# Performance work log

Measured on AMD Instinct MI355X. Metric: run time of the kernel, lower is better.

Reference implementation:

```python
import jax, jax.numpy as jnp
import numpy as np

N_ATOMS = 131072
N_MOLS = 4096
D = 128
N_DEPTH = 128
EPS = 1e-07
MEMBERSHIPS = np.array([(-1.645, 0.283), (-1.08, 0.17), (-0.739, 0.134), (-0.468, 0.118),
                        (-0.228, 0.114), (0.0, 0.114), (0.228, 0.114), (0.468, 0.118),
                        (0.739, 0.134), (1.08, 0.17), (1.645, 0.283)], dtype=np.float32)


def setup_inputs() -> dict:
    key = jax.random.key(0)
    k1, k2, k3, k4 = jax.random.split(key, 4)
    x = jax.random.normal(k1, (N_ATOMS, D), dtype=jnp.float32)
    atom_split = jnp.sort(jax.random.randint(k2, (N_ATOMS,), 0, N_MOLS)).astype(jnp.int64)
    W = jax.random.normal(k3, (D * 11, N_DEPTH), dtype=jnp.float32) * 0.02
    b = jax.random.normal(k4, (N_DEPTH,), dtype=jnp.float32) * 0.02
    return {"x": x, "atom_split": atom_split, "W": W, "b": b}


def reference(x, atom_split, W, b):
    means = jnp.asarray(MEMBERSHIPS[:, 0])          # [11]
    stds = jnp.asarray(MEMBERSHIPS[:, 1])           # [11]
    log_norm = jnp.log(stds * np.sqrt(2.0 * np.pi)) # [11]
    # Normal log_prob: -0.5*((x-m)/s)^2 - log(s*sqrt(2pi)); dist_max = log_prob(m) = -log_norm
    z = (x[:, :, None] - means) / stds              # [N, D, 11]
    logp = -0.5 * z * z - log_norm
    out = logp / (-log_norm)                        # divide by log_prob at mean
    out = (out + EPS) / (jnp.sum(out, axis=2, keepdims=True) + EPS)
    out = out.reshape(-1, D * 11)                   # [N, D*11]
    mols = jax.ops.segment_sum(out, atom_split, num_segments=N_MOLS)  # [M, D*11]
    return jnp.tanh(mols @ W + b)                   # [M, n_depth]
```

## Files before the change

### kernel.cpp

```cpp
#include <hip/hip_runtime.h>
#include <math.h>

#define N_ATOMS 131072
#define N_MOLS  4096
#define DFEAT   128
#define NK      11
#define KDIM3   384
#define N_DEPTH 128
#define EPS_F   1e-7f
#define MPB     4

__constant__ float c_means[NK] = {-1.645f, -1.08f, -0.739f, -0.468f, -0.228f,
                                  0.0f, 0.228f, 0.468f, 0.739f, 1.08f, 1.645f};
__constant__ float c_stds[NK]  = {0.283f, 0.17f, 0.134f, 0.118f, 0.114f,
                                  0.114f, 0.114f, 0.118f, 0.134f, 0.17f, 0.283f};


__global__ __launch_bounds__(256) void wxform_offsets_kernel(
    const float* __restrict__ W,
    const int*   __restrict__ split,
    float*       __restrict__ Bt,
    int*         __restrict__ offsets) {
  const int bid = blockIdx.x;
  const int tid = threadIdx.x;
  if (bid < 192) {
    int t = bid * 256 + tid;
    int n = t & 127;
    int row = t >> 7;
    int j = row >> 7;
    int d = row & 127;
    float acc = 0.0f;
#pragma unroll
    for (int k = 0; k < NK; ++k) {
      float m = c_means[k], s = c_stds[k];
      float a = 0.5f / (s * s * logf(s * 2.5066282746310002f));
      float coef = (j == 2) ? a
                 : (j == 1) ? (-2.0f * a * m)
                            : fmaf(a, m * m, 1.0f + EPS_F);
      acc = fmaf(coef, W[(size_t)(d * NK + k) * N_DEPTH + n], acc);
    }
    Bt[(size_t)row * N_DEPTH + n] = acc;
  } else {
    int t = (bid - 192) * 256 + tid;
    if (t <= N_MOLS) {
      int lo = 0, hi = N_ATOMS;
      while (lo < hi) { int mid = (lo + hi) >> 1; if (split[mid] < t) lo = mid + 1; else hi = mid; }
      offsets[t] = lo;
    }
  }
}

__global__ __launch_bounds__(256) void fused_sums_gemm_kernel(
    const float* __restrict__ x,
    const int*   __restrict__ offsets,
    const float* __restrict__ Bt,
    const float* __restrict__ bias,
    float*       __restrict__ out) {
  const int tid = threadIdx.x;
  const int m0  = blockIdx.x * MPB;

  __shared__ float As[MPB][KDIM3];
  __shared__ float red[8][32][13];
  float (*comb)[MPB][DFEAT] = (float (*)[MPB][DFEAT])red;

  float C2 = 0.0f, C1 = 0.0f, C0 = 11.0f + EPS_F;
#pragma unroll
  for (int k = 0; k < NK; ++k) {
    float m_ = c_means[k], s_ = c_stds[k];
    float a = 0.5f / (s_ * s_ * logf(s_ * 2.5066282746310002f));
    C2 += a;
    C1 = fmaf(-2.0f * a, m_, C1);
    C0 = fmaf(a, m_ * m_, C0);
  }

  int offs[MPB + 1];
#pragma unroll
  for (int i = 0; i <= MPB; ++i) offs[i] = offsets[m0 + i];

  const int fq = tid & 31;
  const int g  = tid >> 5;

  for (int i = 0; i < MPB; ++i) {
    float Sr[4]   = {0.f, 0.f, 0.f, 0.f};
    float Sxr[4]  = {0.f, 0.f, 0.f, 0.f};
    float Sxxr[4] = {0.f, 0.f, 0.f, 0.f};

    for (int a = offs[i] + g; a < offs[i + 1]; a += 8) {
      float4 v = *(const float4*)&x[(size_t)a * DFEAT + fq * 4];
      float xv[4] = {v.x, v.y, v.z, v.w};
#pragma unroll
      for (int q = 0; q < 4; ++q) {
        float den = fmaf(fmaf(C2, xv[q], C1), xv[q], C0);
        float r   = __builtin_amdgcn_rcpf(den);
        float u   = xv[q] * r;
        Sr[q]  += r;
        Sxr[q] += u;
        Sxxr[q] = fmaf(xv[q], u, Sxxr[q]);
      }
    }

#pragma unroll
    for (int q = 0; q < 4; ++q) {
      red[g][fq][q * 3 + 0] = Sr[q];
      red[g][fq][q * 3 + 1] = Sxr[q];
      red[g][fq][q * 3 + 2] = Sxxr[q];
    }
    __syncthreads();

    for (int t = tid; t < KDIM3; t += 256) {
      int j = t >> 7;
      int f = t & 127;
      int q = f >> 2, fi = f & 3;
      float s = 0.0f;
#pragma unroll
      for (int gg = 0; gg < 8; ++gg) s += red[gg][q][fi * 3 + j];
      As[i][t] = s;
    }
    __syncthreads();
  }

  const int n = tid & 127;
  const int h = tid >> 7;
  const int kbase = h * (KDIM3 / 2);

  float acc[MPB] = {0.f, 0.f, 0.f, 0.f};
  for (int kk = 0; kk < KDIM3 / 2; kk += 4) {
    int k = kbase + kk;
    float b0 = Bt[(size_t)(k + 0) * N_DEPTH + n];
    float b1 = Bt[(size_t)(k + 1) * N_DEPTH + n];
    float b2 = Bt[(size_t)(k + 2) * N_DEPTH + n];
    float b3 = Bt[(size_t)(k + 3) * N_DEPTH + n];
#pragma unroll
    for (int i = 0; i < MPB; ++i) {
      float4 av = *(const float4*)&As[i][k];
      acc[i] = fmaf(av.x, b0, acc[i]);
      acc[i] = fmaf(av.y, b1, acc[i]);
      acc[i] = fmaf(av.z, b2, acc[i]);
      acc[i] = fmaf(av.w, b3, acc[i]);
    }
  }

#pragma unroll
  for (int i = 0; i < MPB; ++i) comb[h][i][n] = acc[i];
  __syncthreads();

#pragma unroll
  for (int off = 0; off < (MPB * DFEAT) / 256; ++off) {
    int idx = off * 256 + tid;
    int i  = idx >> 7;
    int nn = idx & 127;
    float v = comb[0][i][nn] + comb[1][i][nn] + bias[nn];
    out[(size_t)(m0 + i) * N_DEPTH + nn] = tanhf(v);
  }
}

extern "C" void kernel_launch(void* const* d_in, const int* in_sizes, int n_in,
                              void* d_out, int out_size, void* d_ws, size_t ws_size,
                              hipStream_t stream) {
  const float* x     = (const float*)d_in[0];
  const int*   split = (const int*)d_in[1];
  const float* W     = (const float*)d_in[2];
  const float* bias  = (const float*)d_in[3];
  float* out = (float*)d_out;

  float* Bt      = (float*)d_ws;
  int*   offsets = (int*)((char*)d_ws + (size_t)KDIM3 * N_DEPTH * 4);

  wxform_offsets_kernel<<<dim3(192 + 17), dim3(256), 0, stream>>>(W, split, Bt, offsets);
  fused_sums_gemm_kernel<<<dim3(N_MOLS / MPB), dim3(256), 0, stream>>>(x, offsets, Bt, bias, out);
}
```

Baseline: 119.1 us.

## Process eight molecules per block with a flat atom loop and predicated accumulation

Raises molecules per block from 4 to 8 and replaces the per-molecule atom loop with one flat loop over all atoms of the block's molecules. Each atom is routed to its molecule by comparing its index against the segment offsets, then accumulated into a per-thread register array of 8x12 partial sums. Loads are unrolled by two to expose more memory parallelism, and launch bounds request two blocks per CU. The aim is to remove the short, unbalanced per-molecule loops and the barriers between them, and to reuse each Bt load across more molecules. The cost is heavy register pressure, per-atom select or branch work across eight accumulators, and half as many blocks to spread over the GPU.

```diff
diff --git a/kernel.cpp b/kernel.cpp
--- a/kernel.cpp
+++ b/kernel.cpp
@@ -8,7 +8,7 @@
 #define KDIM3   384
 #define N_DEPTH 128
 #define EPS_F   1e-7f
-#define MPB     4
+#define MPB     8
 
 __constant__ float c_means[NK] = {-1.645f, -1.08f, -0.739f, -0.468f, -0.228f,
                                   0.0f, 0.228f, 0.468f, 0.739f, 1.08f, 1.645f};
@@ -50,7 +50,7 @@
   }
 }
 
-__global__ __launch_bounds__(256) void fused_sums_gemm_kernel(
+__global__ __launch_bounds__(256, 2) void fused_sums_gemm_kernel(
     const float* __restrict__ x,
     const int*   __restrict__ offsets,
     const float* __restrict__ Bt,
@@ -80,40 +80,62 @@
   const int fq = tid & 31;
   const int g  = tid >> 5;
 
-  for (int i = 0; i < MPB; ++i) {
-    float Sr[4]   = {0.f, 0.f, 0.f, 0.f};
-    float Sxr[4]  = {0.f, 0.f, 0.f, 0.f};
-    float Sxxr[4] = {0.f, 0.f, 0.f, 0.f};
+  float acc[MPB][12];
+#pragma unroll
+  for (int i = 0; i < MPB; ++i)
+#pragma unroll
+    for (int j = 0; j < 12; ++j) acc[i][j] = 0.0f;
 
-    for (int a = offs[i] + g; a < offs[i + 1]; a += 8) {
-      float4 v = *(const float4*)&x[(size_t)a * DFEAT + fq * 4];
-      float xv[4] = {v.x, v.y, v.z, v.w};
+  const int base = offs[0], endA = offs[MPB];
+
+  auto proc = [&](float4 v, int a) {
+    float xv[4] = {v.x, v.y, v.z, v.w};
+    float rr[4], uu[4];
 #pragma unroll
-      for (int q = 0; q < 4; ++q) {
-        float den = fmaf(fmaf(C2, xv[q], C1), xv[q], C0);
-        float r   = __builtin_amdgcn_rcpf(den);
-        float u   = xv[q] * r;
-        Sr[q]  += r;
-        Sxr[q] += u;
-        Sxxr[q] = fmaf(xv[q], u, Sxxr[q]);
+    for (int q = 0; q < 4; ++q) {
+      float den = fmaf(fmaf(C2, xv[q], C1), xv[q], C0);
+      rr[q] = __builtin_amdgcn_rcpf(den);
+      uu[q] = xv[q] * rr[q];
+    }
+    int mid = 0;
+#pragma unroll
+    for (int j = 1; j < MPB; ++j) mid += (a >= offs[j]) ? 1 : 0;
+#pragma unroll
+    for (int i = 0; i < MPB; ++i)
+      if (mid == i) {
+#pragma unroll
+        for (int q = 0; q < 4; ++q) {
+          acc[i][3 * q + 0] += rr[q];
+          acc[i][3 * q + 1] += uu[q];
+          acc[i][3 * q + 2] = fmaf(xv[q], uu[q], acc[i][3 * q + 2]);
+        }
       }
-    }
+  };
+
+  int a = base + g;
+  for (; a + 8 < endA; a += 16) {
+    float4 v0 = *(const float4*)&x[(size_t)a * DFEAT + fq * 4];
+    float4 v1 = *(const float4*)&x[(size_t)(a + 8) * DFEAT + fq * 4];
+    proc(v0, a);
+    proc(v1, a + 8);
+  }
+  if (a < endA) {
+    float4 v = *(const float4*)&x[(size_t)a * DFEAT + fq * 4];
+    proc(v, a);
+  }
 
 #pragma unroll
-    for (int q = 0; q < 4; ++q) {
-      red[g][fq][q * 3 + 0] = Sr[q];
-      red[g][fq][q * 3 + 1] = Sxr[q];
-      red[g][fq][q * 3 + 2] = Sxxr[q];
-    }
+  for (int i = 0; i < MPB; ++i) {
+#pragma unroll
+    for (int j = 0; j < 12; ++j) red[g][fq][j] = acc[i][j];
     __syncthreads();
-
     for (int t = tid; t < KDIM3; t += 256) {
-      int j = t >> 7;
+      int comp = t >> 7;
       int f = t & 127;
       int q = f >> 2, fi = f & 3;
       float s = 0.0f;
 #pragma unroll
-      for (int gg = 0; gg < 8; ++gg) s += red[gg][q][fi * 3 + j];
+      for (int gg = 0; gg < 8; ++gg) s += red[gg][q][fi * 3 + comp];
       As[i][t] = s;
     }
     __syncthreads();
@@ -123,7 +145,11 @@
   const int h = tid >> 7;
   const int kbase = h * (KDIM3 / 2);
 
-  float acc[MPB] = {0.f, 0.f, 0.f, 0.f};
+  float pacc[MPB];
+#pragma unroll
+  for (int i = 0; i < MPB; ++i) pacc[i] = 0.0f;
+
+#pragma unroll 2
   for (int kk = 0; kk < KDIM3 / 2; kk += 4) {
     int k = kbase + kk;
     float b0 = Bt[(size_t)(k + 0) * N_DEPTH + n];
@@ -133,15 +159,15 @@
 #pragma unroll
     for (int i = 0; i < MPB; ++i) {
       float4 av = *(const float4*)&As[i][k];
-      acc[i] = fmaf(av.x, b0, acc[i]);
-      acc[i] = fmaf(av.y, b1, acc[i]);
-      acc[i] = fmaf(av.z, b2, acc[i]);
-      acc[i] = fmaf(av.w, b3, acc[i]);
+      pacc[i] = fmaf(av.x, b0, pacc[i]);
+      pacc[i] = fmaf(av.y, b1, pacc[i]);
+      pacc[i] = fmaf(av.z, b2, pacc[i]);
+      pacc[i] = fmaf(av.w, b3, pacc[i]);
     }
   }
 
 #pragma unroll
-  for (int i = 0; i < MPB; ++i) comb[h][i][n] = acc[i];
+  for (int i = 0; i < MPB; ++i) comb[h][i][n] = pacc[i];
   __syncthreads();
 
 #pragma unroll
```

New measurement: 184.2 us. 54.6% more time.

## Assign one wavefront per molecule and reduce sums with shuffles instead of LDS

Applied to the files above, without the earlier changes.

The fused kernel now runs 512 threads handling 8 molecules per block. Each 64-lane wavefront owns one molecule, with the two half-waves taking alternating atoms and the loop unrolled by two. The per-molecule loop of LDS reductions with two block barriers each is replaced by a single cross-half shuffle and one barrier. The GEMM phase splits K four ways across the block. This removes barrier-heavy serial per-molecule reduction, but makes load balance depend on each molecule's atom count and raises register and block-size pressure.

```diff
diff --git a/kernel.cpp b/kernel.cpp
--- a/kernel.cpp
+++ b/kernel.cpp
@@ -8,7 +8,8 @@
 #define KDIM3   384
 #define N_DEPTH 128
 #define EPS_F   1e-7f
-#define MPB     4
+#define MPB     8
+#define TPB     512
 
 __constant__ float c_means[NK] = {-1.645f, -1.08f, -0.739f, -0.468f, -0.228f,
                                   0.0f, 0.228f, 0.468f, 0.739f, 1.08f, 1.645f};
@@ -50,7 +51,7 @@
   }
 }
 
-__global__ __launch_bounds__(256) void fused_sums_gemm_kernel(
+__global__ __launch_bounds__(TPB) void fused_sums_gemm_kernel(
     const float* __restrict__ x,
     const int*   __restrict__ offsets,
     const float* __restrict__ Bt,
@@ -60,8 +61,7 @@
   const int m0  = blockIdx.x * MPB;
 
   __shared__ float As[MPB][KDIM3];
-  __shared__ float red[8][32][13];
-  float (*comb)[MPB][DFEAT] = (float (*)[MPB][DFEAT])red;
+  __shared__ float comb[4][MPB][DFEAT];
 
   float C2 = 0.0f, C1 = 0.0f, C0 = 11.0f + EPS_F;
 #pragma unroll
@@ -73,58 +73,76 @@
     C0 = fmaf(a, m_ * m_, C0);
   }
 
-  int offs[MPB + 1];
+  const int w    = tid >> 6;
+  const int lane = tid & 63;
+  const int fq   = lane & 31;
+  const int h    = lane >> 5;
+
+  const int start = offsets[m0 + w];
+  const int end   = offsets[m0 + w + 1];
+
+  float Sr[4]   = {0.f, 0.f, 0.f, 0.f};
+  float Sxr[4]  = {0.f, 0.f, 0.f, 0.f};
+  float Sxxr[4] = {0.f, 0.f, 0.f, 0.f};
+
+  int a = start + h;
+  for (; a + 2 < end; a += 4) {
+    float4 v0 = *(const float4*)&x[(size_t)a * DFEAT + fq * 4];
+    float4 v1 = *(const float4*)&x[(size_t)(a + 2) * DFEAT + fq * 4];
+    float xv0[4] = {v0.x, v0.y, v0.z, v0.w};
+    float xv1[4] = {v1.x, v1.y, v1.z, v1.w};
 #pragma unroll
-  for (int i = 0; i <= MPB; ++i) offs[i] = offsets[m0 + i];
-
-  const int fq = tid & 31;
-  const int g  = tid >> 5;
-
-  for (int i = 0; i < MPB; ++i) {
-    float Sr[4]   = {0.f, 0.f, 0.f, 0.f};
-    float Sxr[4]  = {0.f, 0.f, 0.f, 0.f};
-    float Sxxr[4] = {0.f, 0.f, 0.f, 0.f};
-
-    for (int a = offs[i] + g; a < offs[i + 1]; a += 8) {
-      float4 v = *(const float4*)&x[(size_t)a * DFEAT + fq * 4];
-      float xv[4] = {v.x, v.y, v.z, v.w};
+    for (int q = 0; q < 4; ++q) {
+      float den0 = fmaf(fmaf(C2, xv0[q], C1), xv0[q], C0);
+      float den1 = fmaf(fmaf(C2, xv1[q], C1), xv1[q], C0);
+      float r0 = __builtin_amdgcn_rcpf(den0);
+      float r1 = __builtin_amdgcn_rcpf(den1);
+      float u0 = xv0[q] * r0;
+      float u1 = xv1[q] * r1;
+      Sr[q]  += r0 + r1;
+      Sxr[q] += u0 + u1;
+      Sxxr[q] = fmaf(xv0[q], u0, Sxxr[q]);
+      Sxxr[q] = fmaf(xv1[q], u1, Sxxr[q]);
+    }
+  }
+  for (; a < end; a += 2) {
+    float4 v = *(const float4*)&x[(size_t)a * DFEAT + fq * 4];
+    float xv[4] = {v.x, v.y, v.z, v.w};
 #pragma unroll
-      for (int q = 0; q < 4; ++q) {
-        float den = fmaf(fmaf(C2, xv[q], C1), xv[q], C0);
-        float r   = __builtin_amdgcn_rcpf(den);
-        float u   = xv[q] * r;
-        Sr[q]  += r;
-        Sxr[q] += u;
-        Sxxr[q] = fmaf(xv[q], u, Sxxr[q]);
-      }
+    for (int q = 0; q < 4; ++q) {
+      float den = fmaf(fmaf(C2, xv[q], C1), xv[q], C0);
+      float r   = __builtin_amdgcn_rcpf(den);
+      float u   = xv[q] * r;
+      Sr[q]  += r;
+      Sxr[q] += u;
+      Sxxr[q] = fmaf(xv[q], u, Sxxr[q]);
     }
+  }
 
 #pragma unroll
-    for (int q = 0; q < 4; ++q) {
-      red[g][fq][q * 3 + 0] = Sr[q];
-      red[g][fq][q * 3 + 1] = Sxr[q];
-      red[g][fq][q * 3 + 2] = Sxxr[q];
-    }
-    __syncthreads();
-
-    for (int t = tid; t < KDIM3; t += 256) {
-      int j = t >> 7;
-      int f = t & 127;
-      int q = f >> 2, fi = f & 3;
-      float s = 0.0f;
-#pragma unroll
-      for (int gg = 0; gg < 8; ++gg) s += red[gg][q][fi * 3 + j];
-      As[i][t] = s;
-    }
-    __syncthreads();
+  for (int q = 0; q < 4; ++q) {
+    Sr[q]   += __shfl_xor(Sr[q],   32, 64);
+    Sxr[q]  += __shfl_xor(Sxr[q],  32, 64);
+    Sxxr[q] += __shfl_xor(Sxxr[q], 32, 64);
   }
 
-  const int n = tid & 127;
-  const int h = tid >> 7;
-  const int kbase = h * (KDIM3 / 2);
+  if (h == 0) {
+    *(float4*)&As[w][fq * 4]             = make_float4(Sr[0],  Sr[1],  Sr[2],  Sr[3]);
+    *(float4*)&As[w][DFEAT + fq * 4]     = make_float4(Sxr[0], Sxr[1], Sxr[2], Sxr[3]);
+    *(float4*)&As[w][2 * DFEAT + fq * 4] = make_float4(Sxxr[0],Sxxr[1],Sxxr[2],Sxxr[3]);
+  }
+  __syncthreads();
 
-  float acc[MPB] = {0.f, 0.f, 0.f, 0.f};
-  for (int kk = 0; kk < KDIM3 / 2; kk += 4) {
+  const int n  = tid & 127;
+  const int hh = tid >> 7;
+  const int kbase = hh * (KDIM3 / 4);
+
+  float pacc[MPB];
+#pragma unroll
+  for (int i = 0; i < MPB; ++i) pacc[i] = 0.0f;
+
+#pragma unroll 2
+  for (int kk = 0; kk < KDIM3 / 4; kk += 4) {
     int k = kbase + kk;
     float b0 = Bt[(size_t)(k + 0) * N_DEPTH + n];
     float b1 = Bt[(size_t)(k + 1) * N_DEPTH + n];
@@ -133,23 +151,24 @@
 #pragma unroll
     for (int i = 0; i < MPB; ++i) {
       float4 av = *(const float4*)&As[i][k];
-      acc[i] = fmaf(av.x, b0, acc[i]);
-      acc[i] = fmaf(av.y, b1, acc[i]);
-      acc[i] = fmaf(av.z, b2, acc[i]);
-      acc[i] = fmaf(av.w, b3, acc[i]);
+      pacc[i] = fmaf(av.x, b0, pacc[i]);
+      pacc[i] = fmaf(av.y, b1, pacc[i]);
+      pacc[i] = fmaf(av.z, b2, pacc[i]);
+      pacc[i] = fmaf(av.w, b3, pacc[i]);
     }
   }
 
 #pragma unroll
-  for (int i = 0; i < MPB; ++i) comb[h][i][n] = acc[i];
+  for (int i = 0; i < MPB; ++i) comb[hh][i][n] = pacc[i];
   __syncthreads();
 
 #pragma unroll
-  for (int off = 0; off < (MPB * DFEAT) / 256; ++off) {
-    int idx = off * 256 + tid;
+  for (int off = 0; off < (MPB * DFEAT) / TPB; ++off) {
+    int idx = off * TPB + tid;
     int i  = idx >> 7;
     int nn = idx & 127;
-    float v = comb[0][i][nn] + comb[1][i][nn] + bias[nn];
+    float v = comb[0][i][nn] + comb[1][i][nn] + comb[2][i][nn] + comb[3][i][nn]
+            + bias[nn];
     out[(size_t)(m0 + i) * N_DEPTH + nn] = tanhf(v);
   }
 }
@@ -167,5 +186,5 @@
   int*   offsets = (int*)((char*)d_ws + (size_t)KDIM3 * N_DEPTH * 4);
 
   wxform_offsets_kernel<<<dim3(192 + 17), dim3(256), 0, stream>>>(W, split, Bt, offsets);
-  fused_sums_gemm_kernel<<<dim3(N_MOLS / MPB), dim3(256), 0, stream>>>(x, offsets, Bt, bias, out);
+  fused_sums_gemm_kernel<<<dim3(N_MOLS / MPB), dim3(TPB), 0, stream>>>(x, offsets, Bt, bias, out);
 }
```

After: 113.4 us. 1.05x faster.
